# Performance work log

Hardware: AMD Instinct MI355X
Metric: run time of the kernel (lower is better)

Reference implementation:

```python
import jax, jax.numpy as jnp
import numpy as np

D = 4; R = 12; C = 32
P = 2 * R + 1            # 25 fine patch
N = P * P                # 625
MEM_R = 12; MEM_P = 2 * MEM_R + 1
K = 20; DIL_INT = 16


def local_correlation(ft, fr, rad, dil):
    """Zero-padded local correlation (SpatialCorrelationSampler, kernel=1).
    ft, fr: (b,c,h,w) -> (b,Pp,Pp,h,w) with Pp=2*rad+1, patch dilation dil."""
    b, c, h, w = ft.shape
    Pp = 2 * rad + 1
    pad = rad * dil
    frp = jnp.pad(fr, ((0, 0), (0, 0), (pad, pad), (pad, pad)))
    rows = (jnp.arange(Pp)[:, None] * dil + jnp.arange(h)[None, :]).reshape(-1)
    cols = (jnp.arange(Pp)[:, None] * dil + jnp.arange(w)[None, :]).reshape(-1)
    g = frp[:, :, rows, :][:, :, :, cols].reshape(b, c, Pp, h, Pp, w)
    return jnp.einsum('bchw,bcyhxw->byxhw', ft, g)


def bilinear_sample(img, py, px):
    """Bilinear sample img (b,c,H,W) at float coords py/px (broadcastable shape S);
    zero outside the image. Returns (b,c,*S)."""
    b, c, H, W = img.shape
    y0f = jnp.floor(py); x0f = jnp.floor(px)
    wy = py - y0f; wx = px - x0f
    y0 = y0f.astype(jnp.int32); x0 = x0f.astype(jnp.int32)

    def tap(yi, xi, wgt):
        valid = (yi >= 0) & (yi < H) & (xi >= 0) & (xi < W)
        v = img[:, :, jnp.clip(yi, 0, H - 1), jnp.clip(xi, 0, W - 1)]
        return v * (wgt * valid)[None, None]

    return (tap(y0, x0, (1 - wy) * (1 - wx)) + tap(y0, x0 + 1, (1 - wy) * wx)
            + tap(y0 + 1, x0, wy * (1 - wx)) + tap(y0 + 1, x0 + 1, wy * wx))


def _topk_dim1(corr, k):
    # corr: (b,N,hw); torch.topk(dim=1, sorted=True) equivalent
    vals, idx = jax.lax.top_k(corr.transpose(0, 2, 1), k)   # (b,hw,k)
    return vals.transpose(0, 2, 1), idx                      # (b,k,hw), (b,hw,k)


def _long_ref(ft, fr, q, dirate):
    b, c, h, w = ft.shape
    # coarse dilated correlation -> softmax -> soft-argmax expected offset
    corr_c = local_correlation(ft, fr, MEM_R, dirate).reshape(b, MEM_P * MEM_P, h * w)
    attn = jax.nn.softmax(corr_c, axis=1).reshape(b, MEM_P, MEM_P, h, w)
    d = jnp.arange(-MEM_R, MEM_R + 1, dtype=ft.dtype)
    off_y = jnp.einsum('byxhw,y->bhw', attn, d) * dirate
    off_x = jnp.einsum('byxhw,x->bhw', attn, d) * dirate
    # deform_im2col with PxP kernel: sample fr at (r+dy+off_y, c+dx+off_x)
    dtap = jnp.arange(-R, R + 1, dtype=ft.dtype)
    py = dtap[:, None, None, None] + (jnp.arange(h, dtype=ft.dtype)[:, None] + off_y[0])[None, None]
    px = dtap[None, :, None, None] + (jnp.arange(w, dtype=ft.dtype)[None, :] + off_x[0])[None, None]
    col = bilinear_sample(fr, py, px)                        # (b,c,P,P,h,w)
    corr = jnp.einsum('bchw,bcyxhw->byxhw', ft, col).reshape(b, N, h * w)
    vals, idx = _topk_dim1(corr, K)
    # process_long_image_uf_topk: shift offsets by decoded top-k displacement, 1-tap bilinear
    dr = (idx[0] // 25 - 12).reshape(h, w, K).transpose(2, 0, 1).astype(ft.dtype)  # (K,h,w)
    dc = (idx[0] % 25 - 12).reshape(h, w, K).transpose(2, 0, 1).astype(ft.dtype)
    py2 = jnp.arange(h, dtype=ft.dtype)[None, :, None] + off_y[0][None] + dr
    px2 = jnp.arange(w, dtype=ft.dtype)[None, None, :] + off_x[0][None] + dc
    imgs = bilinear_sample(q, py2, px2)                      # (b,C,K,h,w)
    return vals, imgs.reshape(b, q.shape[1], K, h * w)


def _short_ref(ft, fr, q):
    b, c, h, w = ft.shape
    corr = local_correlation(ft, fr, R, 1).reshape(b, N, h * w)
    vals, idx = _topk_dim1(corr, K)
    # process_short_image_uf_topk: integer gather q[:, :, r+dr, c+dc] (zero-padded)
    dr = (idx[0] // 25 - 12).reshape(h, w, K).transpose(2, 0, 1)   # (K,h,w) int
    dc = (idx[0] % 25 - 12).reshape(h, w, K).transpose(2, 0, 1)
    qp = jnp.pad(q, ((0, 0), (0, 0), (R, R), (R, R)))
    yi = jnp.arange(h)[None, :, None] + dr + R
    xi = jnp.arange(w)[None, None, :] + dc + R
    imgs = qp[:, :, yi, xi]                                  # (b,C,K,h,w)
    return vals, imgs.reshape(b, q.shape[1], K, h * w)


def _forward(feats_r, feats_t, quantized_r, ref_index, current_ind):
    ref_index = np.asarray(ref_index)
    current_ind = int(current_ind)
    gaps = current_ind - ref_index
    nsearch = int(np.sum(gaps > DIL_INT))
    dirates = [int(min(4, g // DIL_INT + 1)) for g in gaps if g > DIL_INT]
    nref = feats_r.shape[0]
    b, c, h, w = feats_t.shape
    # prep(): subsample labels by D (C=32 channels, one_hot skipped)
    qr = [quantized_r[i][:, :, ::D, ::D].astype(feats_t.dtype) for i in range(nref)]
    vals_all, imgs_all = [], []
    for i in range(nsearch):
        v, im = _long_ref(feats_t, feats_r[i], qr[i], dirates[i])
        vals_all.append(v); imgs_all.append(im)
    for i in range(nsearch, nref):
        v, im = _short_ref(feats_t, feats_r[i], qr[i])
        vals_all.append(v); imgs_all.append(im)
    attn = jax.nn.softmax(jnp.concatenate(vals_all, axis=1), axis=1)  # (b, nref*K, hw)
    imgs = jnp.concatenate(imgs_all, axis=2)                          # (b, C, nref*K, hw)
    return jnp.einsum('bkp,bckp->bcp', attn, imgs).reshape(b, qr[0].shape[1], h, w)


def setup_inputs():
    key = jax.random.key(0)
    k1, k2, k3 = jax.random.split(key, 3)
    feats_r = jax.random.normal(k1, (3, 1, 64, 48, 48), dtype=jnp.float32)
    feats_t = jax.random.normal(k2, (1, 64, 48, 48), dtype=jnp.float32)
    quantized_r = jax.random.uniform(k3, (3, 1, 32, 192, 192), dtype=jnp.float32)
    # gaps vs current_ind=60: 20 (>16 -> long ref, dirate=2), 10, 5 (short refs)
    ref_index = np.array([40, 50, 55], dtype=np.int64)
    current_ind = 60
    return {"feats_r": feats_r, "feats_t": feats_t, "quantized_r": quantized_r,
            "ref_index": ref_index, "current_ind": current_ind}


def reference(feats_r, feats_t, quantized_r, ref_index, current_ind):
    return _forward(feats_r, feats_t, quantized_r, ref_index, current_ind)
```

## Files before the change

kernel.cpp:

```cpp
#include <hip/hip_runtime.h>
#include <math.h>

#define HW 48
#define NPIX 2304
#define CF 64
#define CQ 32
#define RAD 12
#define PP 25
#define NTAP 625
#define KTOP 20
#define DILINT 16
#define QW 192
#define CSTRIDE 640
#define NPB 6
#define NC 30
#define LROW 68
#define DGS 28


__device__ inline int read_ref_index(const void* rip, int r) {
    const long long* p64 = (const long long*)rip;
    long long v0 = p64[0];
    if (v0 >= 0 && v0 < 1000000) return (int)p64[r];
    return ((const int*)rip)[r];
}

__device__ inline int get_dil(const void* refIdx, const void* curInd, int r,
                              bool* isLong) {
    int cur = ((const int*)curInd)[0];
    int gap = cur - read_ref_index(refIdx, r);
    *isLong = gap > DILINT;
    return *isLong ? min(4, gap / DILINT + 1) : 1;
}

__global__ void prep_kernel(const float* __restrict__ fr,
                            const float* __restrict__ ft,
                            const float* __restrict__ q, int nref,
                            float* __restrict__ ftT,
                            float* __restrict__ frT,
                            float* __restrict__ qrT) {
    int i = blockIdx.x * blockDim.x + threadIdx.x;
    int tft = NPIX * CF;
    int tfr = nref * NPIX * CF;
    int tqr = nref * NPIX * CQ;
    if (i < tft) {
        int p = i >> 6, c = i & 63;
        ftT[i] = ft[c * NPIX + p];
    } else if (i < tft + tfr) {
        int j = i - tft;
        int rr = j / (NPIX * CF);
        int rem = j % (NPIX * CF);
        int p = rem >> 6, c = rem & 63;
        frT[j] = fr[((size_t)rr * CF + c) * NPIX + p];
    } else if (i < tft + tfr + tqr) {
        int j = i - tft - tfr;
        int rr = j / (NPIX * CQ);
        int rem = j % (NPIX * CQ);
        int p = rem >> 5, c = rem & 31;
        int y = p / HW, x = p % HW;
        qrT[j] = q[(((size_t)rr * CQ + c) * QW + 4 * y) * QW + 4 * x];
    }
}

__global__ __launch_bounds__(256) void corr_band(
    const float* __restrict__ ftT, const float* __restrict__ frT,
    const void* __restrict__ refIdx, const void* __restrict__ curInd,
    float* __restrict__ corr) {
    __shared__ float lrow[NC * LROW];

    int tid = threadIdx.x;
    int bx = blockIdx.x % 9;
    int y = blockIdx.x / 9;
    int r = blockIdx.y;

    bool isLong;
    int dil = get_dil(refIdx, curInd, r, &isLong);
    int nb = (dil == 3) ? 9 : 8;
    if (bx >= nb) return;

    int m = bx % dil, grp = bx / dil;
    int npr = HW / dil;

    int T = tid;
    bool active = T < NPB * PP;
    int j = active ? T / PP : 0;
    int dxi = active ? T - PP * j : 0;
    int xoff = grp * NPB + j;
    bool pvalid = active && (xoff < npr);
    int xj = m + dil * xoff;
    int pj = pvalid ? (y * HW + xj) : 0;
    int lc = j + dxi;

    float4 fq[16];
    const float4* fp = (const float4*)(ftT + (size_t)pj * CF);
#pragma unroll
    for (int i = 0; i < 16; ++i) fq[i] = fp[i];

    const float* frb = frT + (size_t)r * NPIX * CF;
    float* outb = corr + ((size_t)r * NPIX + pj) * CSTRIDE + dxi;
    int gc0 = m + dil * (grp * NPB - RAD);

    for (int dy = 0; dy < PP; ++dy) {
        int yy = y + dil * (dy - RAD);
        if (yy < 0 || yy >= HW) {
            if (pvalid) outb[dy * PP] = 0.f;
            continue;
        }
        for (int k = tid; k < NC * 16; k += 256) {
            int col = k >> 4, sub = k & 15;
            int gc = gc0 + dil * col;
            float4 v = {0.f, 0.f, 0.f, 0.f};
            if (gc >= 0 && gc < HW)
                v = *(const float4*)(frb + ((size_t)yy * HW + gc) * CF + sub * 4);
            *(float4*)(lrow + col * LROW + sub * 4) = v;
        }
        __syncthreads();
        if (pvalid) {
            const float* bp = lrow + lc * LROW;
            float s = 0.f;
#pragma unroll
            for (int i = 0; i < 16; ++i) {
                float4 b = *(const float4*)(bp + 4 * i);
                s += fq[i].x * b.x + fq[i].y * b.y + fq[i].z * b.z + fq[i].w * b.w;
            }
            outb[dy * PP] = s;
        }
        __syncthreads();
    }
}

__global__ __launch_bounds__(192) void corr_fuse(
    const float* __restrict__ ftT, const float* __restrict__ frT,
    const float* __restrict__ qrT, const float* __restrict__ corr,
    const void* __restrict__ refIdx, const void* __restrict__ curInd,
    int nref, float* __restrict__ out) {
    __shared__ float dgw_s[3][27 * DGS];
    __shared__ float valsL[96];
    __shared__ int   topiL[96];
    __shared__ float accL[3][64];
    __shared__ float ssmL[3][64];
    __shared__ float offL[3][2];

    int tid = threadIdx.x;
    int wid = tid >> 6, lane = tid & 63;
    int p = blockIdx.x;
    int y = p / HW, x = p % HW;
    int r = wid;

    bool isLong;
    int dil = get_dil(refIdx, curInd, r, &isLong);
    float oy = 0.f, ox = 0.f;

    const float* cb = corr + ((size_t)r * NPIX + p) * CSTRIDE;
    float creg[10];
#pragma unroll
    for (int jj = 0; jj < 10; ++jj) {
        int t = lane + 64 * jj;
        creg[jj] = (t < NTAP) ? cb[t] : -INFINITY;
    }

    if (isLong) {
        float M = -INFINITY;
#pragma unroll
        for (int jj = 0; jj < 10; ++jj) M = fmaxf(M, creg[jj]);
#pragma unroll
        for (int s = 32; s; s >>= 1) M = fmaxf(M, __shfl_xor(M, s, 64));
        float s0 = 0.f, sy = 0.f, sx = 0.f;
#pragma unroll
        for (int jj = 0; jj < 10; ++jj) {
            int t = lane + 64 * jj;
            if (t < NTAP) {
                float e = expf(creg[jj] - M);
                int dy = t / PP - RAD, dx = t % PP - RAD;
                s0 += e; sy += e * (float)dy; sx += e * (float)dx;
            }
        }
#pragma unroll
        for (int s = 32; s; s >>= 1) {
            s0 += __shfl_xor(s0, s, 64);
            sy += __shfl_xor(sy, s, 64);
            sx += __shfl_xor(sx, s, 64);
        }
        oy = sy / s0 * (float)dil;
        ox = sx / s0 * (float)dil;
        if (lane == 0) { offL[r][0] = oy; offL[r][1] = ox; }
    }
    __syncthreads();

    for (int rr = 0; rr < nref; ++rr) {
        bool rrLong;
        get_dil(refIdx, curInd, rr, &rrLong);
        if (!rrLong) continue;
        float roy = offL[rr][0], rox = offL[rr][1];
        float fy = (float)y + roy, fx = (float)x + rox;
        int iy0 = (int)floorf(fy), ix0 = (int)floorf(fx);

        int cs = tid & 15;
        int g2 = tid >> 4;
        float4 fqc = ((const float4*)(ftT + (size_t)p * CF))[cs];
        const float* frb = frT + (size_t)rr * NPIX * CF;
        float* dgw = dgw_s[rr];
        int colbase = ix0 - RAD;
        for (int a = 0; a < 26; ++a) {
            int yy = iy0 - RAD + a;
            bool yok = (yy >= 0 && yy < HW);
            const float* rowp = frb + (size_t)(yok ? yy : 0) * (HW * CF);
#pragma unroll
            for (int i = 0; i < 3; ++i) {
                int lc2 = 12 * i + g2;
                int xx2 = colbase + lc2;
                int xs = min(max(xx2, 0), HW - 1);
                float s = 0.f;
                if (yok && lc2 < 26) {
                    float4 b = *(const float4*)(rowp + xs * CF + 4 * cs);
                    s = fqc.x * b.x + fqc.y * b.y + fqc.z * b.z + fqc.w * b.w;
                    s = (xx2 >= 0 && xx2 < HW) ? s : 0.f;
                }
                s += __shfl_xor(s, 1, 64);
                s += __shfl_xor(s, 2, 64);
                s += __shfl_xor(s, 4, 64);
                s += __shfl_xor(s, 8, 64);
                if (cs == 0 && lc2 < 26) dgw[a * DGS + lc2] = s;
            }
        }
    }
    __syncthreads();

    if (isLong) {
        float fy = (float)y + oy, fx = (float)x + ox;
        float fy0 = floorf(fy), fx0 = floorf(fx);
        float wy = fy - fy0, wx = fx - fx0;
        const float* dgw = dgw_s[r];
        float w00 = (1.f - wy) * (1.f - wx), w01 = (1.f - wy) * wx;
        float w10 = wy * (1.f - wx), w11 = wy * wx;
#pragma unroll
        for (int jj = 0; jj < 10; ++jj) {
            int t = lane + 64 * jj;
            if (t < NTAP) {
                int a = t / PP, bcol = t % PP;
                creg[jj] = w00 * dgw[a * DGS + bcol] + w01 * dgw[a * DGS + bcol + 1] +
                           w10 * dgw[(a + 1) * DGS + bcol] + w11 * dgw[(a + 1) * DGS + bcol + 1];
            }
        }
    }

    for (int k = 0; k < KTOP; ++k) {
        float bv = creg[0]; int bt = lane;
#pragma unroll
        for (int jj = 1; jj < 10; ++jj) {
            int t = lane + 64 * jj;
            if (creg[jj] > bv) { bv = creg[jj]; bt = t; }
        }
#pragma unroll
        for (int s = 32; s; s >>= 1) {
            float ov = __shfl_xor(bv, s, 64);
            int ot = __shfl_xor(bt, s, 64);
            if (ov > bv || (ov == bv && ot < bt)) { bv = ov; bt = ot; }
        }
        if (lane == 0) { valsL[r * KTOP + k] = bv; topiL[r * KTOP + k] = bt; }
        if ((bt & 63) == lane) {
            int jj2 = bt >> 6;
#pragma unroll
            for (int jj = 0; jj < 10; ++jj)
                if (jj == jj2) creg[jj] = -INFINITY;
        }
    }
    __syncthreads();

    int c = lane & 31, h = lane >> 5;
    int nk = nref * KTOP;
    float m = -INFINITY;
    for (int k = 0; k < nk; ++k) m = fmaxf(m, valsL[k]);

    float ssum = 0.f, acc = 0.f;
    const float* qb = qrT + (size_t)r * NPIX * CQ;
    for (int k2 = 0; k2 < KTOP / 2; ++k2) {
        int k = r * KTOP + h * (KTOP / 2) + k2;
        float e = expf(valsL[k] - m);
        ssum += e;
        int id = topiL[k];
        int dr = id / PP - RAD, dc = id % PP - RAD;
        float img = 0.f;
        if (isLong) {
            float py = (float)y + oy + (float)dr;
            float px = (float)x + ox + (float)dc;
            float fy0 = floorf(py), fx0 = floorf(px);
            int y0 = (int)fy0, x0 = (int)fx0;
            float wy = py - fy0, wx = px - fx0;
            float w00 = (1.f - wy) * (1.f - wx), w01 = (1.f - wy) * wx;
            float w10 = wy * (1.f - wx), w11 = wy * wx;
            if (y0 >= 0 && y0 < HW && x0 >= 0 && x0 < HW)
                img += w00 * qb[(y0 * HW + x0) * CQ + c];
            if (y0 >= 0 && y0 < HW && x0 + 1 >= 0 && x0 + 1 < HW)
                img += w01 * qb[(y0 * HW + x0 + 1) * CQ + c];
            if (y0 + 1 >= 0 && y0 + 1 < HW && x0 >= 0 && x0 < HW)
                img += w10 * qb[((y0 + 1) * HW + x0) * CQ + c];
            if (y0 + 1 >= 0 && y0 + 1 < HW && x0 + 1 >= 0 && x0 + 1 < HW)
                img += w11 * qb[((y0 + 1) * HW + x0 + 1) * CQ + c];
        } else {
            int yy = y + dr, xx = x + dc;
            if (yy >= 0 && yy < HW && xx >= 0 && xx < HW)
                img = qb[(yy * HW + xx) * CQ + c];
        }
        acc += e * img;
    }
    accL[wid][lane] = acc;
    ssmL[wid][lane] = ssum;
    __syncthreads();

    if (wid == 0) {
        float ta = 0.f, ts = 0.f;
        for (int w = 0; w < nref; ++w) { ta += accL[w][lane]; ts += ssmL[w][lane]; }
        ta += __shfl_xor(ta, 32, 64);
        ts += __shfl_xor(ts, 32, 64);
        if (h == 0) out[(size_t)c * NPIX + p] = ta / ts;
    }
}

extern "C" void kernel_launch(void* const* d_in, const int* in_sizes, int n_in,
                              void* d_out, int out_size, void* d_ws, size_t ws_size,
                              hipStream_t stream) {
    const float* fr = (const float*)d_in[0];
    const float* ft = (const float*)d_in[1];
    const float* q  = (const float*)d_in[2];
    const void* refIdx = d_in[3];
    const void* curInd = d_in[4];
    int nref = in_sizes[0] / (CF * NPIX);

    float* ws  = (float*)d_ws;
    float* ftT = ws;
    float* frT = ftT + (size_t)NPIX * CF;
    float* qrT = frT + (size_t)nref * NPIX * CF;
    float* corr = qrT + (size_t)nref * NPIX * CQ;

    int total = NPIX * CF + nref * NPIX * CF + nref * NPIX * CQ;
    prep_kernel<<<(total + 255) / 256, 256, 0, stream>>>(fr, ft, q, nref, ftT, frT, qrT);
    corr_band<<<dim3(HW * 9, nref), 256, 0, stream>>>(ftT, frT, refIdx, curInd, corr);
    corr_fuse<<<dim3(NPIX), 64 * nref, 0, stream>>>(ftT, frT, qrT, corr, refIdx, curInd,
                                                    nref, (float*)d_out);
}
```

Measured before the change: 118.9 us.

## Widen corr_band pixel tiles, pack top-k keys, pair deform rows, shuffle max

Several independent changes: corr_band now covers 10 pixels per block (NPB 10, NC 34) with the block count per row derived from the dilation, so fewer blocks are launched. The deformable-window correlation processes two rows per iteration with interleaved shuffle reductions to expose more memory-level parallelism. Top-k selection packs each value and its index into a single sortable 64-bit key, so each round needs one compare per element plus a 64-bit shuffle-max instead of separate value/index shuffles. The softmax max is computed with a wave reduction instead of a serial loop over shared memory. The risks are higher register pressure from the 64-bit keys and doubled row loads, and the tie-breaking behaviour of the packed keys must match the earlier code.

After: 125.9 us. 5.9% more time.

```diff
diff --git a/kernel.cpp b/kernel.cpp
--- a/kernel.cpp
+++ b/kernel.cpp
@@ -12,10 +12,11 @@
 #define DILINT 16
 #define QW 192
 #define CSTRIDE 640
-#define NPB 6
-#define NC 30
+#define NPB 10
+#define NC 34
 #define LROW 68
 #define DGS 28
+#define NBX 8
 
 
 __device__ inline int read_ref_index(const void* rip, int r) {
@@ -31,6 +32,13 @@
     int gap = cur - read_ref_index(refIdx, r);
     *isLong = gap > DILINT;
     return *isLong ? min(4, gap / DILINT + 1) : 1;
+}
+
+__device__ inline unsigned long long shfl_xor_u64(unsigned long long v, int m) {
+    unsigned lo = (unsigned)v, hi = (unsigned)(v >> 32);
+    lo = (unsigned)__shfl_xor((int)lo, m, 64);
+    hi = (unsigned)__shfl_xor((int)hi, m, 64);
+    return ((unsigned long long)hi << 32) | lo;
 }
 
 __global__ void prep_kernel(const float* __restrict__ fr,
@@ -69,17 +77,17 @@
     __shared__ float lrow[NC * LROW];
 
     int tid = threadIdx.x;
-    int bx = blockIdx.x % 9;
-    int y = blockIdx.x / 9;
+    int bx = blockIdx.x % NBX;
+    int y = blockIdx.x / NBX;
     int r = blockIdx.y;
 
     bool isLong;
     int dil = get_dil(refIdx, curInd, r, &isLong);
-    int nb = (dil == 3) ? 9 : 8;
+    int npr = HW / dil;
+    int nb = dil * ((npr + NPB - 1) / NPB);
     if (bx >= nb) return;
 
     int m = bx % dil, grp = bx / dil;
-    int npr = HW / dil;
 
     int T = tid;
     bool active = T < NPB * PP;
@@ -201,26 +209,37 @@
         const float* frb = frT + (size_t)rr * NPIX * CF;
         float* dgw = dgw_s[rr];
         int colbase = ix0 - RAD;
-        for (int a = 0; a < 26; ++a) {
-            int yy = iy0 - RAD + a;
-            bool yok = (yy >= 0 && yy < HW);
-            const float* rowp = frb + (size_t)(yok ? yy : 0) * (HW * CF);
+        for (int a0 = 0; a0 < 26; a0 += 2) {
+            int yy0 = iy0 - RAD + a0;
+            int yy1 = yy0 + 1;
+            bool yok0 = (yy0 >= 0 && yy0 < HW);
+            bool yok1 = (yy1 >= 0 && yy1 < HW);
+            const float* rowp0 = frb + (size_t)(yok0 ? yy0 : 0) * (HW * CF);
+            const float* rowp1 = frb + (size_t)(yok1 ? yy1 : 0) * (HW * CF);
 #pragma unroll
             for (int i = 0; i < 3; ++i) {
                 int lc2 = 12 * i + g2;
                 int xx2 = colbase + lc2;
                 int xs = min(max(xx2, 0), HW - 1);
-                float s = 0.f;
-                if (yok && lc2 < 26) {
-                    float4 b = *(const float4*)(rowp + xs * CF + 4 * cs);
-                    s = fqc.x * b.x + fqc.y * b.y + fqc.z * b.z + fqc.w * b.w;
-                    s = (xx2 >= 0 && xx2 < HW) ? s : 0.f;
+                bool xok = (xx2 >= 0 && xx2 < HW);
+                float4 b0 = *(const float4*)(rowp0 + xs * CF + 4 * cs);
+                float4 b1 = *(const float4*)(rowp1 + xs * CF + 4 * cs);
+                float s0v = fqc.x * b0.x + fqc.y * b0.y + fqc.z * b0.z + fqc.w * b0.w;
+                float s1v = fqc.x * b1.x + fqc.y * b1.y + fqc.z * b1.z + fqc.w * b1.w;
+                s0v = (yok0 && xok) ? s0v : 0.f;
+                s1v = (yok1 && xok) ? s1v : 0.f;
+                s0v += __shfl_xor(s0v, 1, 64);
+                s1v += __shfl_xor(s1v, 1, 64);
+                s0v += __shfl_xor(s0v, 2, 64);
+                s1v += __shfl_xor(s1v, 2, 64);
+                s0v += __shfl_xor(s0v, 4, 64);
+                s1v += __shfl_xor(s1v, 4, 64);
+                s0v += __shfl_xor(s0v, 8, 64);
+                s1v += __shfl_xor(s1v, 8, 64);
+                if (cs == 0 && lc2 < 26) {
+                    dgw[a0 * DGS + lc2] = s0v;
+                    dgw[(a0 + 1) * DGS + lc2] = s1v;
                 }
-                s += __shfl_xor(s, 1, 64);
-                s += __shfl_xor(s, 2, 64);
-                s += __shfl_xor(s, 4, 64);
-                s += __shfl_xor(s, 8, 64);
-                if (cs == 0 && lc2 < 26) dgw[a * DGS + lc2] = s;
             }
         }
     }
@@ -244,33 +263,42 @@
         }
     }
 
+    unsigned long long key[10];
+#pragma unroll
+    for (int jj = 0; jj < 10; ++jj) {
+        float v = creg[jj] + 0.0f;
+        unsigned u = __float_as_uint(v);
+        u = (u & 0x80000000u) ? ~u : (u | 0x80000000u);
+        unsigned it = 0xFFFFFFFFu - (unsigned)(lane + 64 * jj);
+        key[jj] = ((unsigned long long)u << 32) | it;
+    }
+
     for (int k = 0; k < KTOP; ++k) {
-        float bv = creg[0]; int bt = lane;
-#pragma unroll
-        for (int jj = 1; jj < 10; ++jj) {
-            int t = lane + 64 * jj;
-            if (creg[jj] > bv) { bv = creg[jj]; bt = t; }
-        }
+        unsigned long long bk = key[0];
+#pragma unroll
+        for (int jj = 1; jj < 10; ++jj) bk = (key[jj] > bk) ? key[jj] : bk;
 #pragma unroll
         for (int s = 32; s; s >>= 1) {
-            float ov = __shfl_xor(bv, s, 64);
-            int ot = __shfl_xor(bt, s, 64);
-            if (ov > bv || (ov == bv && ot < bt)) { bv = ov; bt = ot; }
-        }
-        if (lane == 0) { valsL[r * KTOP + k] = bv; topiL[r * KTOP + k] = bt; }
-        if ((bt & 63) == lane) {
-            int jj2 = bt >> 6;
-#pragma unroll
-            for (int jj = 0; jj < 10; ++jj)
-                if (jj == jj2) creg[jj] = -INFINITY;
-        }
+            unsigned long long ok = shfl_xor_u64(bk, s);
+            bk = (ok > bk) ? ok : bk;
+        }
+        if (lane == 0) {
+            unsigned u = (unsigned)(bk >> 32);
+            unsigned bits = (u & 0x80000000u) ? (u ^ 0x80000000u) : ~u;
+            valsL[r * KTOP + k] = __uint_as_float(bits);
+            topiL[r * KTOP + k] = (int)(0xFFFFFFFFu - (unsigned)(bk & 0xFFFFFFFFu));
+        }
+#pragma unroll
+        for (int jj = 0; jj < 10; ++jj)
+            if (key[jj] == bk) key[jj] = 0ull;
     }
     __syncthreads();
 
     int c = lane & 31, h = lane >> 5;
     int nk = nref * KTOP;
-    float m = -INFINITY;
-    for (int k = 0; k < nk; ++k) m = fmaxf(m, valsL[k]);
+    float m = (lane < nk) ? valsL[lane] : -INFINITY;
+#pragma unroll
+    for (int s = 32; s; s >>= 1) m = fmaxf(m, __shfl_xor(m, s, 64));
 
     float ssum = 0.f, acc = 0.f;
     const float* qb = qrT + (size_t)r * NPIX * CQ;
@@ -335,7 +363,7 @@
 
     int total = NPIX * CF + nref * NPIX * CF + nref * NPIX * CQ;
     prep_kernel<<<(total + 255) / 256, 256, 0, stream>>>(fr, ft, q, nref, ftT, frT, qrT);
-    corr_band<<<dim3(HW * 9, nref), 256, 0, stream>>>(ftT, frT, refIdx, curInd, corr);
+    corr_band<<<dim3(HW * NBX, nref), 256, 0, stream>>>(ftT, frT, refIdx, curInd, corr);
     corr_fuse<<<dim3(NPIX), 64 * nref, 0, stream>>>(ftT, frT, qrT, corr, refIdx, curInd,
                                                     nref, (float*)d_out);
 }
```
